# Optimization experiments

Measured on AMD Instinct MI355X. Metric: run time of the kernel, lower is better.

The kernel has to match this reference:

```python
import jax, jax.numpy as jnp
import numpy as np
from math import sqrt

DIM = 256
NUM_HEADS = 4
GROUPS = 32  # min(256//4, 32)
EPS = 1e-6


def group_norm(x, gamma, beta, groups=GROUPS, eps=EPS):
    # x: (B, C, H, W); normalize per group over (C//G, H, W)
    B, C, H, W = x.shape
    xg = x.reshape(B, groups, C // groups, H, W)
    mu = jnp.mean(xg, axis=(2, 3, 4), keepdims=True)
    var = jnp.var(xg, axis=(2, 3, 4), keepdims=True)
    xn = ((xg - mu) * jax.lax.rsqrt(var + eps)).reshape(B, C, H, W)
    return xn * gamma[None, :, None, None] + beta[None, :, None, None]


def lin_on_channel(x, W, bias):
    # torch Linear on channel dim: W is (out, in)
    return jnp.einsum('bchw,oc->bohw', x, W) + bias[None, :, None, None]


def setup_inputs() -> dict:
    key = jax.random.key(0)
    ks = jax.random.split(key, 14)
    B, C, H, W = 16, DIM, 32, 32
    s = 1.0 / sqrt(DIM)
    return {
        'a': jax.random.normal(ks[0], (B, C, H, W), jnp.float32),
        'b': jax.random.normal(ks[1], (B, C, H, W), jnp.float32),
        'Wq': jax.random.normal(ks[2], (DIM, DIM), jnp.float32) * s,
        'bq': jnp.zeros((DIM,), jnp.float32),
        'Wk': jax.random.normal(ks[3], (DIM, DIM), jnp.float32) * s,
        'bk': jnp.zeros((DIM,), jnp.float32),
        'Wv': jax.random.normal(ks[4], (DIM, DIM), jnp.float32) * s,
        'bv': jnp.zeros((DIM,), jnp.float32),
        'Wp': jax.random.normal(ks[5], (DIM, DIM), jnp.float32) * s,
        'bp': jnp.zeros((DIM,), jnp.float32),
        'gnA_w': jnp.ones((DIM,), jnp.float32),
        'gnA_b': jnp.zeros((DIM,), jnp.float32),
        'gnB_w': jnp.ones((DIM,), jnp.float32),
        'gnB_b': jnp.zeros((DIM,), jnp.float32),
    }


def reference(a, b, Wq, bq, Wk, bk, Wv, bv, Wp, bp, gnA_w, gnA_b, gnB_w, gnB_b):
    B, C, H, W = a.shape
    _, _, H2, W2 = b.shape
    dh = DIM // NUM_HEADS
    skip_b = b
    an = group_norm(a, gnA_w, gnA_b)
    bn = group_norm(b, gnB_w, gnB_b)
    q = lin_on_channel(bn, Wq, bq).reshape(B, NUM_HEADS, dh, H2, W2)
    k = lin_on_channel(an, Wk, bk).reshape(B, NUM_HEADS, dh, H, W)
    # NOTE: value uses pre-posemb but post-groupnorm 'a' (same as an here)
    v = lin_on_channel(an, Wv, bv).reshape(B, NUM_HEADS, dh, H, W)
    scores = jnp.einsum('bhdxy,bhdij->bhxyij', q, k) / sqrt(DIM)
    attn = jax.nn.softmax(scores.reshape(B, NUM_HEADS, H2, W2, H * W), axis=-1)
    attn = attn.reshape(B, NUM_HEADS, H2, W2, H, W)
    h = jnp.einsum('bhxyij,bhdij->bhdxy', attn, v).reshape(B, DIM, H2, W2)
    h = lin_on_channel(h, Wp, bp)
    ret = skip_b + h
    return ret / sqrt(2.0)
```

## Files before the change

### kernel.cpp

```cpp
#include <hip/hip_runtime.h>
#include <hip/hip_bf16.h>

#define BSZ 16
#define CDIM 256
#define NPIX 1024
#define NH 4
#define DHD 64
#define EPSV 1e-6f
#define QSCALE 0.0625f
#define INV_SQRT2 0.70710678118654752440f

typedef __attribute__((ext_vector_type(4))) float f32x4;
typedef __attribute__((ext_vector_type(8))) __bf16 bf16x8;
typedef __attribute__((ext_vector_type(4))) __bf16 bf16x4;

#define OFF_WBF   0UL
#define OFF_STATS (512UL*1024)
#define OFF_ANT   (1024UL*1024)
#define OFF_BNT   (OFF_ANT + 8UL*1024*1024)
#define OFF_Q     (OFF_BNT + 8UL*1024*1024)
#define OFF_K     (OFF_Q   + 8UL*1024*1024)
#define OFF_V     (OFF_K   + 8UL*1024*1024)
#define OFF_H     (OFF_V   + 8UL*1024*1024)

__global__ __launch_bounds__(256) void prep_w(const float* __restrict__ Wq, const float* __restrict__ Wk,
                                              const float* __restrict__ Wv, const float* __restrict__ Wp,
                                              __bf16* __restrict__ out){
  int m = blockIdx.y;
  const float* src = (m==0)?Wq:(m==1)?Wk:(m==2)?Wv:Wp;
  float scale = (m==0)?QSCALE:1.0f;
  int idx = (blockIdx.x*256 + threadIdx.x)*4;
  float4 v = *(const float4*)(src + idx);
  bf16x4 o;
  o[0]=(__bf16)(v.x*scale); o[1]=(__bf16)(v.y*scale);
  o[2]=(__bf16)(v.z*scale); o[3]=(__bf16)(v.w*scale);
  *(bf16x4*)(out + m*65536 + idx) = o;
}

__global__ __launch_bounds__(256) void gn_stats(const float* __restrict__ xa, const float* __restrict__ xb,
                                                float2* __restrict__ stats){
  int bx = blockIdx.x;
  int t = bx >> 9; int rem = bx & 511; int bb = rem >> 5; int g = rem & 31;
  const float* src = (t ? xb : xa) + ((size_t)(bb*CDIM + g*8))*NPIX;
  float s = 0.f, ss = 0.f;
  for (int i = 0; i < 8; i++){
    float4 v = *(const float4*)(src + (threadIdx.x + 256*i)*4);
    s  += v.x+v.y+v.z+v.w;
    ss += v.x*v.x+v.y*v.y+v.z*v.z+v.w*v.w;
  }
  __shared__ float rs[256], rss[256];
  rs[threadIdx.x]=s; rss[threadIdx.x]=ss; __syncthreads();
  for (int st=128; st>0; st>>=1){
    if (threadIdx.x < st){ rs[threadIdx.x]+=rs[threadIdx.x+st]; rss[threadIdx.x]+=rss[threadIdx.x+st]; }
    __syncthreads();
  }
  if (threadIdx.x==0){
    float mean = rs[0]*(1.0f/8192.0f);
    float var  = rss[0]*(1.0f/8192.0f) - mean*mean;
    stats[(t*16+bb)*32+g] = make_float2(mean, rsqrtf(var + EPSV));
  }
}

__global__ __launch_bounds__(256) void norm_t(const float* __restrict__ xa, const float* __restrict__ xb,
                                              const float* __restrict__ gAw, const float* __restrict__ gAb,
                                              const float* __restrict__ gBw, const float* __restrict__ gBb,
                                              const float2* __restrict__ stats,
                                              __bf16* __restrict__ ant, __bf16* __restrict__ bnt){
  __shared__ __align__(16) __bf16 T[64][72];
  int t = blockIdx.z;
  const float* src = t ? xb : xa;
  const float* gw  = t ? gBw : gAw;
  const float* gb  = t ? gBb : gAb;
  __bf16* dst = t ? bnt : ant;
  int bb = blockIdx.y >> 2, cblk = blockIdx.y & 3;
  int p0 = blockIdx.x*64, c0 = cblk*64;
  int tid = threadIdx.x;
  int r16 = tid>>4, c4 = tid&15;
  for (int pass=0; pass<4; pass++){
    int cl = r16 + 16*pass;
    int c  = c0 + cl;
    float2 ms = stats[(t*16+bb)*32 + (c>>3)];
    float sc  = ms.y * gw[c];
    float off = gb[c] - ms.x*sc;
    float4 v = *(const float4*)(src + ((size_t)(bb*CDIM + c))*NPIX + p0 + c4*4);
    T[c4*4+0][cl] = (__bf16)(v.x*sc+off);
    T[c4*4+1][cl] = (__bf16)(v.y*sc+off);
    T[c4*4+2][cl] = (__bf16)(v.z*sc+off);
    T[c4*4+3][cl] = (__bf16)(v.w*sc+off);
  }
  __syncthreads();
  for (int pass=0; pass<2; pass++){
    int slot = tid + 256*pass;
    int pl = slot>>3, ch = slot&7;
    *(float4*)(dst + ((size_t)(bb*NPIX + p0 + pl))*CDIM + c0 + ch*8) = *(float4*)&T[pl][ch*8];
  }
}

__global__ __launch_bounds__(256,2) void gemm_qk(const __bf16* __restrict__ Wqk,
    const __bf16* __restrict__ bnt, const __bf16* __restrict__ ant,
    const float* __restrict__ bq, const float* __restrict__ bk,
    __bf16* __restrict__ qws, __bf16* __restrict__ kws){
  __shared__ __align__(16) __bf16 As[128][76], Bs[128][76];
  int i0 = blockIdx.x;
  int wg = (i0&7)*64 + (i0>>3);
  int my = wg&3, nx = wg>>2;
  int m0 = my*128, n0 = nx*128;
  const __bf16* Bm = (my<2) ? bnt : ant;
  int tid=threadIdx.x, lane=tid&63, wid=tid>>6;
  int wm=(wid>>1)*64, wn=(wid&1)*64, g=lane>>4, c=lane&15;
  f32x4 acc[4][4];
  #pragma unroll
  for (int i=0;i<4;i++)
    #pragma unroll
    for (int j=0;j<4;j++) acc[i][j]=(f32x4){0.f,0.f,0.f,0.f};
  int row[4], ch[4];
  #pragma unroll
  for (int i=0;i<4;i++){ int slot=tid+256*i; row[i]=slot>>3; ch[i]=slot&7; }
  for (int k0=0; k0<256; k0+=64){
    #pragma unroll
    for (int i=0;i<4;i++){
      *(float4*)&As[row[i]][ch[i]*8] = *(const float4*)(Wqk + (size_t)(m0+row[i])*256 + k0 + ch[i]*8);
      *(float4*)&Bs[row[i]][ch[i]*8] = *(const float4*)(Bm  + (size_t)(n0+row[i])*256 + k0 + ch[i]*8);
    }
    __syncthreads();
    #pragma unroll
    for (int ks=0;ks<2;ks++){
      bf16x8 af[4], bfr[4];
      #pragma unroll
      for (int i=0;i<4;i++) af[i]  = *(bf16x8*)&As[wm+i*16+c][ks*32+g*8];
      #pragma unroll
      for (int j=0;j<4;j++) bfr[j] = *(bf16x8*)&Bs[wn+j*16+c][ks*32+g*8];
      #pragma unroll
      for (int i=0;i<4;i++)
        #pragma unroll
        for (int j=0;j<4;j++)
          acc[i][j] = __builtin_amdgcn_mfma_f32_16x16x32_bf16(af[i], bfr[j], acc[i][j],0,0,0);
    }
    __syncthreads();
  }
  const float* bias = (my<2)? bq : bk;
  float bscale = (my<2)? QSCALE : 1.0f;
  __bf16* dst = (my<2)? qws : kws;
  int mbase = (my<2)? m0 : (m0-256);
  #pragma unroll
  for (int fm=0;fm<4;fm++){
    #pragma unroll
    for (int fn=0;fn<4;fn++){
      int o = mbase + wm + fm*16 + g*4;
      int n = n0 + wn + fn*16 + c;
      int bb=n>>10, p=n&1023;
      f32x4 v = acc[fm][fn];
      bf16x4 pk;
      #pragma unroll
      for (int r=0;r<4;r++) pk[r] = (__bf16)(v[r] + bias[o+r]*bscale);
      *(bf16x4*)(dst + ((size_t)((bb*4+(o>>6))*1024 + p))*64 + (o&63)) = pk;
    }
  }
}

__global__ __launch_bounds__(256,2) void gemm_sw(const __bf16* __restrict__ A,
    const __bf16* __restrict__ Wn, const float* __restrict__ bias,
    void* __restrict__ dst_, const float* __restrict__ skip, int mode){
  __shared__ __align__(16) __bf16 As[128][76], Bs[64][76];
  int i0 = blockIdx.x;
  int wg = (i0&7)*64 + (i0>>3);
  int ny = wg&3, mx = wg>>2;
  int m0 = mx*128, n0 = ny*64;
  int tid=threadIdx.x, lane=tid&63, wid=tid>>6;
  int wm=(wid>>1)*64, wn=(wid&1)*32, g=lane>>4, c=lane&15;
  f32x4 acc[4][2];
  #pragma unroll
  for (int i=0;i<4;i++)
    #pragma unroll
    for (int j=0;j<2;j++) acc[i][j]=(f32x4){0.f,0.f,0.f,0.f};
  int rowA[4], chA[4], rowB[2], chB[2];
  #pragma unroll
  for (int i=0;i<4;i++){ int slot=tid+256*i; rowA[i]=slot>>3; chA[i]=slot&7; }
  #pragma unroll
  for (int i=0;i<2;i++){ int slot=tid+256*i; rowB[i]=slot>>3; chB[i]=slot&7; }
  for (int k0=0; k0<256; k0+=64){
    #pragma unroll
    for (int i=0;i<4;i++)
      *(float4*)&As[rowA[i]][chA[i]*8] = *(const float4*)(A  + (size_t)(m0+rowA[i])*256 + k0 + chA[i]*8);
    #pragma unroll
    for (int i=0;i<2;i++)
      *(float4*)&Bs[rowB[i]][chB[i]*8] = *(const float4*)(Wn + (size_t)(n0+rowB[i])*256 + k0 + chB[i]*8);
    __syncthreads();
    #pragma unroll
    for (int ks=0;ks<2;ks++){
      bf16x8 af[4], bfr[2];
      #pragma unroll
      for (int i=0;i<4;i++) af[i]  = *(bf16x8*)&As[wm+i*16+c][ks*32+g*8];
      #pragma unroll
      for (int j=0;j<2;j++) bfr[j] = *(bf16x8*)&Bs[wn+j*16+c][ks*32+g*8];
      #pragma unroll
      for (int i=0;i<4;i++)
        #pragma unroll
        for (int j=0;j<2;j++)
          acc[i][j] = __builtin_amdgcn_mfma_f32_16x16x32_bf16(af[i], bfr[j], acc[i][j],0,0,0);
    }
    __syncthreads();
  }
  #pragma unroll
  for (int fm=0;fm<4;fm++){
    #pragma unroll
    for (int fn=0;fn<2;fn++){
      int m = m0 + wm + fm*16 + g*4;
      int n = n0 + wn + fn*16 + c;
      int bb=m>>10, p=m&1023;
      f32x4 v = acc[fm][fn];
      if (mode==0){
        float bv = bias[n];
        bf16x4 pk;
        #pragma unroll
        for (int r=0;r<4;r++) pk[r] = (__bf16)(v[r] + bv);
        *(bf16x4*)((__bf16*)dst_ + ((size_t)((bb*4+(n>>6))*64 + (n&63)))*1024 + p) = pk;
      } else {
        float bv = bias[n];
        size_t addr = (size_t)(bb*256 + n)*1024 + p;
        float4 sk = *(const float4*)(skip + addr);
        float4 ov;
        ov.x=(sk.x+v[0]+bv)*INV_SQRT2; ov.y=(sk.y+v[1]+bv)*INV_SQRT2;
        ov.z=(sk.z+v[2]+bv)*INV_SQRT2; ov.w=(sk.w+v[3]+bv)*INV_SQRT2;
        *(float4*)((float*)dst_ + addr) = ov;
      }
    }
  }
}

__global__ __launch_bounds__(256,4) void attn_k(const __bf16* __restrict__ q, const __bf16* __restrict__ k,
                                                const __bf16* __restrict__ v, __bf16* __restrict__ hout){
  __shared__ __align__(16) __bf16 Kl[64][76], Vl[64][76], Pl[4][16][76];
  __shared__ float l_lds[4][16];
  int i0 = blockIdx.x;
  int wg = (i0&7)*128 + (i0>>3);
  int bh = wg>>4, qblk = wg&15;
  int tid = threadIdx.x, lane = tid&63, w = tid>>6;
  int g = lane>>4, c = lane&15;
  int bb = bh>>2, h = bh&3;
  const __bf16* qbase = q + (size_t)bh*NPIX*DHD;
  const __bf16* kbase = k + (size_t)bh*NPIX*DHD;
  const __bf16* vbase = v + (size_t)bh*DHD*NPIX;

  int qrow = qblk*64 + w*16 + c;
  bf16x8 qf0 = *(const bf16x8*)(qbase + (size_t)qrow*64 +      g*8);
  bf16x8 qf1 = *(const bf16x8*)(qbase + (size_t)qrow*64 + 32 + g*8);

  f32x4 oacc[4];
  #pragma unroll
  for (int i=0;i<4;i++) oacc[i] = (f32x4){0.f,0.f,0.f,0.f};
  float l0=0.f, l1=0.f, l2=0.f, l3=0.f;

  int srow[2], sch[2];
  #pragma unroll
  for (int i=0;i<2;i++){ int slot=tid+256*i; srow[i]=slot>>3; sch[i]=slot&7; }

  for (int kt=0; kt<16; kt++){
    #pragma unroll
    for (int i=0;i<2;i++){
      *(float4*)&Kl[srow[i]][sch[i]*8] = *(const float4*)(kbase + (size_t)(kt*64+srow[i])*64 + sch[i]*8);
      *(float4*)&Vl[srow[i]][sch[i]*8] = *(const float4*)(vbase + (size_t)srow[i]*1024 + kt*64 + sch[i]*8);
    }
    __syncthreads();
    f32x4 s[4];
    #pragma unroll
    for (int fn=0; fn<4; fn++){
      bf16x8 kb0 = *(bf16x8*)&Kl[fn*16 + c][     g*8];
      bf16x8 kb1 = *(bf16x8*)&Kl[fn*16 + c][32 + g*8];
      f32x4 z = (f32x4){0.f,0.f,0.f,0.f};
      z     = __builtin_amdgcn_mfma_f32_16x16x32_bf16(qf0, kb0, z, 0,0,0);
      s[fn] = __builtin_amdgcn_mfma_f32_16x16x32_bf16(qf1, kb1, z, 0,0,0);
    }
    #pragma unroll
    for (int fn=0; fn<4; fn++){
      float p0 = __expf(s[fn][0]); l0 += p0; Pl[w][g*4+0][fn*16+c] = (__bf16)p0;
      float p1 = __expf(s[fn][1]); l1 += p1; Pl[w][g*4+1][fn*16+c] = (__bf16)p1;
      float p2 = __expf(s[fn][2]); l2 += p2; Pl[w][g*4+2][fn*16+c] = (__bf16)p2;
      float p3 = __expf(s[fn][3]); l3 += p3; Pl[w][g*4+3][fn*16+c] = (__bf16)p3;
    }
    bf16x8 pb0 = *(bf16x8*)&Pl[w][c][     g*8];
    bf16x8 pb1 = *(bf16x8*)&Pl[w][c][32 + g*8];
    #pragma unroll
    for (int fm=0; fm<4; fm++){
      bf16x8 va0 = *(bf16x8*)&Vl[fm*16+c][     g*8];
      bf16x8 va1 = *(bf16x8*)&Vl[fm*16+c][32 + g*8];
      oacc[fm] = __builtin_amdgcn_mfma_f32_16x16x32_bf16(va0, pb0, oacc[fm], 0,0,0);
      oacc[fm] = __builtin_amdgcn_mfma_f32_16x16x32_bf16(va1, pb1, oacc[fm], 0,0,0);
    }
    __syncthreads();
  }

  l0 += __shfl_xor(l0,1); l0 += __shfl_xor(l0,2); l0 += __shfl_xor(l0,4); l0 += __shfl_xor(l0,8);
  l1 += __shfl_xor(l1,1); l1 += __shfl_xor(l1,2); l1 += __shfl_xor(l1,4); l1 += __shfl_xor(l1,8);
  l2 += __shfl_xor(l2,1); l2 += __shfl_xor(l2,2); l2 += __shfl_xor(l2,4); l2 += __shfl_xor(l2,8);
  l3 += __shfl_xor(l3,1); l3 += __shfl_xor(l3,2); l3 += __shfl_xor(l3,4); l3 += __shfl_xor(l3,8);
  float lv = (c==0)?l0:(c==1)?l1:(c==2)?l2:l3;
  if (c < 4) l_lds[w][g*4+c] = lv;
  __syncthreads();
  float linv = 1.0f / l_lds[w][c];

  int qg = qblk*64 + w*16 + c;
  #pragma unroll
  for (int fm=0; fm<4; fm++){
    bf16x4 pk;
    #pragma unroll
    for (int r=0;r<4;r++) pk[r] = (__bf16)(oacc[fm][r]*linv);
    *(bf16x4*)(hout + ((size_t)(bb*NPIX + qg))*CDIM + h*64 + fm*16 + g*4) = pk;
  }
}

extern "C" void kernel_launch(void* const* d_in, const int* in_sizes, int n_in,
                              void* d_out, int out_size, void* d_ws, size_t ws_size,
                              hipStream_t stream) {
  const float* xa  = (const float*)d_in[0];
  const float* xb  = (const float*)d_in[1];
  const float* Wq  = (const float*)d_in[2];
  const float* bq  = (const float*)d_in[3];
  const float* Wk  = (const float*)d_in[4];
  const float* bk  = (const float*)d_in[5];
  const float* Wv  = (const float*)d_in[6];
  const float* bv  = (const float*)d_in[7];
  const float* Wp  = (const float*)d_in[8];
  const float* bp  = (const float*)d_in[9];
  const float* gAw = (const float*)d_in[10];
  const float* gAb = (const float*)d_in[11];
  const float* gBw = (const float*)d_in[12];
  const float* gBb = (const float*)d_in[13];

  char* ws = (char*)d_ws;
  __bf16* wbf   = (__bf16*)(ws + OFF_WBF);
  float2* stats = (float2*)(ws + OFF_STATS);
  __bf16* ant   = (__bf16*)(ws + OFF_ANT);
  __bf16* bnt   = (__bf16*)(ws + OFF_BNT);
  __bf16* qws   = (__bf16*)(ws + OFF_Q);
  __bf16* kws   = (__bf16*)(ws + OFF_K);
  __bf16* vws   = (__bf16*)(ws + OFF_V);
  __bf16* hws   = (__bf16*)(ws + OFF_H);

  prep_w<<<dim3(64,4), 256, 0, stream>>>(Wq, Wk, Wv, Wp, wbf);
  gn_stats<<<1024, 256, 0, stream>>>(xa, xb, stats);
  norm_t<<<dim3(16,64,2), 256, 0, stream>>>(xa, xb, gAw, gAb, gBw, gBb, stats, ant, bnt);
  gemm_qk<<<512, 256, 0, stream>>>(wbf, bnt, ant, bq, bk, qws, kws);
  gemm_sw<<<512, 256, 0, stream>>>(ant, wbf + 2*65536, bv, vws, nullptr, 0);
  attn_k<<<1024, 256, 0, stream>>>(qws, kws, vws, hws);
  gemm_sw<<<512, 256, 0, stream>>>(hws, wbf + 3*65536, bp, d_out, xb, 1);
}
```

Before: 182.3 us.

## Double-buffer K/V tiles with async global-to-LDS loads and XOR-swizzled LDS

The attention kernel now stages K and V tiles into two LDS buffers using direct global_load_lds async copies, prefetching the next tile while the current one is computed. This is meant to hide global load latency and drop one barrier per iteration. Padded LDS arrays are replaced by XOR-swizzled layouts for K, V and P to avoid bank conflicts without padding. The final row-sum exchange now uses a lane shuffle instead of an LDS round-trip and barrier. The cost is more LDS for the double buffers, which may lower occupancy.

```diff
diff --git a/kernel.cpp b/kernel.cpp
--- a/kernel.cpp
+++ b/kernel.cpp
@@ -13,6 +13,10 @@
 typedef __attribute__((ext_vector_type(4))) float f32x4;
 typedef __attribute__((ext_vector_type(8))) __bf16 bf16x8;
 typedef __attribute__((ext_vector_type(4))) __bf16 bf16x4;
+
+#define ASYNC16(gp, lp) __builtin_amdgcn_global_load_lds( \
+    (const __attribute__((address_space(1))) void*)(gp),  \
+    (__attribute__((address_space(3))) void*)(lp), 16, 0, 0)
 
 #define OFF_WBF   0UL
 #define OFF_STATS (512UL*1024)
@@ -230,74 +234,92 @@
 
 __global__ __launch_bounds__(256,4) void attn_k(const __bf16* __restrict__ q, const __bf16* __restrict__ k,
                                                 const __bf16* __restrict__ v, __bf16* __restrict__ hout){
-  __shared__ __align__(16) __bf16 Kl[64][76], Vl[64][76], Pl[4][16][76];
-  __shared__ float l_lds[4][16];
+  __shared__ __align__(16) __bf16 Kb[2][4096];
+  __shared__ __align__(16) __bf16 Vb[2][4096];
+  __shared__ __align__(16) __bf16 Pl[4][1024];
   int i0 = blockIdx.x;
   int wg = (i0&7)*128 + (i0>>3);
   int bh = wg>>4, qblk = wg&15;
   int tid = threadIdx.x, lane = tid&63, w = tid>>6;
   int g = lane>>4, c = lane&15;
   int bb = bh>>2, h = bh&3;
+  const char* kbyte = (const char*)(k + (size_t)bh*NPIX*DHD);
+  const char* vbyte = (const char*)(v + (size_t)bh*DHD*NPIX);
   const __bf16* qbase = q + (size_t)bh*NPIX*DHD;
-  const __bf16* kbase = k + (size_t)bh*NPIX*DHD;
-  const __bf16* vbase = v + (size_t)bh*DHD*NPIX;
 
   int qrow = qblk*64 + w*16 + c;
   bf16x8 qf0 = *(const bf16x8*)(qbase + (size_t)qrow*64 +      g*8);
   bf16x8 qf1 = *(const bf16x8*)(qbase + (size_t)qrow*64 + 32 + g*8);
 
+  int srow = w*8 + (lane>>3);
+  int scol = ((lane&7) ^ (lane>>3)) << 4;
+  const char* ks0 = kbyte + srow*128 + scol;
+  const char* vs0 = vbyte + (size_t)srow*2048 + scol;
+
   f32x4 oacc[4];
   #pragma unroll
   for (int i=0;i<4;i++) oacc[i] = (f32x4){0.f,0.f,0.f,0.f};
-  float l0=0.f, l1=0.f, l2=0.f, l3=0.f;
-
-  int srow[2], sch[2];
-  #pragma unroll
-  for (int i=0;i<2;i++){ int slot=tid+256*i; srow[i]=slot>>3; sch[i]=slot&7; }
-
+  float la0=0.f, la1=0.f, la2=0.f, la3=0.f;
+  int cs = (c&7)<<4;
+  char* pw = (char*)&Pl[w][0];
+
+  #define STAGE(buf, kt) { \
+    const char* ks_ = ks0 + (size_t)(kt)*8192; \
+    const char* vs_ = vs0 + (size_t)(kt)*128; \
+    ASYNC16(ks_,          &Kb[buf][w*512]); \
+    ASYNC16(ks_ + 4096,   &Kb[buf][2048 + w*512]); \
+    ASYNC16(vs_,          &Vb[buf][w*512]); \
+    ASYNC16(vs_ + 65536,  &Vb[buf][2048 + w*512]); }
+
+  STAGE(0, 0)
   for (int kt=0; kt<16; kt++){
-    #pragma unroll
-    for (int i=0;i<2;i++){
-      *(float4*)&Kl[srow[i]][sch[i]*8] = *(const float4*)(kbase + (size_t)(kt*64+srow[i])*64 + sch[i]*8);
-      *(float4*)&Vl[srow[i]][sch[i]*8] = *(const float4*)(vbase + (size_t)srow[i]*1024 + kt*64 + sch[i]*8);
-    }
-    __syncthreads();
+    int cur = kt&1;
+    __syncthreads();
+    if (kt<15) STAGE(cur^1, kt+1)
+    const char* KL = (const char*)&Kb[cur][0];
+    const char* VL = (const char*)&Vb[cur][0];
     f32x4 s[4];
     #pragma unroll
     for (int fn=0; fn<4; fn++){
-      bf16x8 kb0 = *(bf16x8*)&Kl[fn*16 + c][     g*8];
-      bf16x8 kb1 = *(bf16x8*)&Kl[fn*16 + c][32 + g*8];
+      int r = fn*16+c;
+      bf16x8 kb0 = *(const bf16x8*)(KL + r*128 + ((     g*16) ^ cs));
+      bf16x8 kb1 = *(const bf16x8*)(KL + r*128 + ((64 + g*16) ^ cs));
       f32x4 z = (f32x4){0.f,0.f,0.f,0.f};
       z     = __builtin_amdgcn_mfma_f32_16x16x32_bf16(qf0, kb0, z, 0,0,0);
       s[fn] = __builtin_amdgcn_mfma_f32_16x16x32_bf16(qf1, kb1, z, 0,0,0);
     }
     #pragma unroll
     for (int fn=0; fn<4; fn++){
-      float p0 = __expf(s[fn][0]); l0 += p0; Pl[w][g*4+0][fn*16+c] = (__bf16)p0;
-      float p1 = __expf(s[fn][1]); l1 += p1; Pl[w][g*4+1][fn*16+c] = (__bf16)p1;
-      float p2 = __expf(s[fn][2]); l2 += p2; Pl[w][g*4+2][fn*16+c] = (__bf16)p2;
-      float p3 = __expf(s[fn][3]); l3 += p3; Pl[w][g*4+3][fn*16+c] = (__bf16)p3;
-    }
-    bf16x8 pb0 = *(bf16x8*)&Pl[w][c][     g*8];
-    bf16x8 pb1 = *(bf16x8*)&Pl[w][c][32 + g*8];
+      int cb = (fn*16+c)*2;
+      float p0 = __expf(s[fn][0]); la0 += p0;
+      float p1 = __expf(s[fn][1]); la1 += p1;
+      float p2 = __expf(s[fn][2]); la2 += p2;
+      float p3 = __expf(s[fn][3]); la3 += p3;
+      *(__bf16*)(pw + (g*4+0)*128 + (cb ^ (((g*4+0)&7)<<4))) = (__bf16)p0;
+      *(__bf16*)(pw + (g*4+1)*128 + (cb ^ (((g*4+1)&7)<<4))) = (__bf16)p1;
+      *(__bf16*)(pw + (g*4+2)*128 + (cb ^ (((g*4+2)&7)<<4))) = (__bf16)p2;
+      *(__bf16*)(pw + (g*4+3)*128 + (cb ^ (((g*4+3)&7)<<4))) = (__bf16)p3;
+    }
+    bf16x8 pb0 = *(const bf16x8*)(pw + c*128 + ((     g*16) ^ cs));
+    bf16x8 pb1 = *(const bf16x8*)(pw + c*128 + ((64 + g*16) ^ cs));
     #pragma unroll
     for (int fm=0; fm<4; fm++){
-      bf16x8 va0 = *(bf16x8*)&Vl[fm*16+c][     g*8];
-      bf16x8 va1 = *(bf16x8*)&Vl[fm*16+c][32 + g*8];
+      int r = fm*16+c;
+      bf16x8 va0 = *(const bf16x8*)(VL + r*128 + ((     g*16) ^ cs));
+      bf16x8 va1 = *(const bf16x8*)(VL + r*128 + ((64 + g*16) ^ cs));
       oacc[fm] = __builtin_amdgcn_mfma_f32_16x16x32_bf16(va0, pb0, oacc[fm], 0,0,0);
       oacc[fm] = __builtin_amdgcn_mfma_f32_16x16x32_bf16(va1, pb1, oacc[fm], 0,0,0);
     }
-    __syncthreads();
-  }
-
-  l0 += __shfl_xor(l0,1); l0 += __shfl_xor(l0,2); l0 += __shfl_xor(l0,4); l0 += __shfl_xor(l0,8);
-  l1 += __shfl_xor(l1,1); l1 += __shfl_xor(l1,2); l1 += __shfl_xor(l1,4); l1 += __shfl_xor(l1,8);
-  l2 += __shfl_xor(l2,1); l2 += __shfl_xor(l2,2); l2 += __shfl_xor(l2,4); l2 += __shfl_xor(l2,8);
-  l3 += __shfl_xor(l3,1); l3 += __shfl_xor(l3,2); l3 += __shfl_xor(l3,4); l3 += __shfl_xor(l3,8);
-  float lv = (c==0)?l0:(c==1)?l1:(c==2)?l2:l3;
-  if (c < 4) l_lds[w][g*4+c] = lv;
-  __syncthreads();
-  float linv = 1.0f / l_lds[w][c];
+  }
+  #undef STAGE
+
+  la0 += __shfl_xor(la0,1); la0 += __shfl_xor(la0,2); la0 += __shfl_xor(la0,4); la0 += __shfl_xor(la0,8);
+  la1 += __shfl_xor(la1,1); la1 += __shfl_xor(la1,2); la1 += __shfl_xor(la1,4); la1 += __shfl_xor(la1,8);
+  la2 += __shfl_xor(la2,1); la2 += __shfl_xor(la2,2); la2 += __shfl_xor(la2,4); la2 += __shfl_xor(la2,8);
+  la3 += __shfl_xor(la3,1); la3 += __shfl_xor(la3,2); la3 += __shfl_xor(la3,4); la3 += __shfl_xor(la3,8);
+  float vsel = ((c&3)==0)? la0 : ((c&3)==1)? la1 : ((c&3)==2)? la2 : la3;
+  float lq = __shfl(vsel, (c>>2)*16 + (c&3));
+  float linv = 1.0f / lq;
 
   int qg = qblk*64 + w*16 + c;
   #pragma unroll
```

Result: faster. 174.5 us (-4.3%).
